# Performance work log

Hardware: AMD Instinct MI355X
Metric: run time of the kernel (lower is better)

## Reference

```python
import jax, jax.numpy as jnp
import numpy as np

B, S, H, I, E = 2, 2048, 1024, 4096, 8


def setup_inputs() -> dict:
    key = jax.random.key(0)
    k1, k2, k3, k4 = jax.random.split(key, 4)
    hidden_states = jax.random.normal(k1, (B, S, H), dtype=jnp.float32)
    # router: nn.Linear(H, E, bias=False) -> weight (E, H)
    Wr = jax.random.normal(k2, (E, H), dtype=jnp.float32) * 0.02
    # per-expert MLP: Linear(H,I) weight (I,H); Linear(I,H) weight (H,I); stacked over E
    W1 = jax.random.normal(k3, (E, I, H), dtype=jnp.float32) * 0.02
    W2 = jax.random.normal(k4, (E, H, I), dtype=jnp.float32) * 0.02
    return {"hidden_states": hidden_states, "Wr": Wr, "W1": W1, "W2": W2}


def reference(hidden_states, Wr, W1, W2):
    b, s, h = hidden_states.shape
    n_exp = Wr.shape[0]
    x = hidden_states.reshape(-1, h)                      # (N, H)
    logits = x @ Wr.T                                     # (N, E)
    probs = jax.nn.softmax(logits, axis=-1)               # (N, E)
    # top_k with k == num_experts: sorted probs descending (one-hot mask then
    # covers every expert, so each expert sees every token; expert i's output is
    # weighted by the i-th largest prob, exactly as the torch code does).
    top_probs, _ = jax.lax.top_k(probs, n_exp)            # (N, E)
    hmid = jnp.einsum('nh,eih->nei', x, W1)               # (N, E, I)
    hmid = jax.nn.gelu(hmid, approximate=False)           # exact erf GELU (torch nn.GELU default)
    yexp = jnp.einsum('nei,ehi->neh', hmid, W2)           # (N, E, H)
    out = jnp.einsum('neh,ne->nh', yexp, top_probs)       # weighted combine
    return out.reshape(b, s, h)
```

## Files before the change

kernel.cpp:

```cpp
#include <hip/hip_runtime.h>
#include <hip/hip_bf16.h>

#define NTOK 4096
#define HD   1024
#define ID   4096
#define NE   8
#define LDH  (NE * ID)

typedef float  floatx4 __attribute__((ext_vector_type(4)));
typedef __bf16 bf16x8  __attribute__((ext_vector_type(8)));
typedef unsigned short u16;

__device__ __forceinline__ u16 f2bf(float f) {
    union { float f; unsigned int i; } c; c.f = f;
    return (u16)((c.i + 0x7fffu + ((c.i >> 16) & 1u)) >> 16);
}

__device__ __forceinline__ void async_copy16(u16* lds, const u16* g) {
    __builtin_amdgcn_global_load_lds(
        (const __attribute__((address_space(1))) void*)g,
        (__attribute__((address_space(3))) void*)lds, 16, 0, 0);
}

__device__ __forceinline__ float gelu_fast(float v) {
    const float u = v * (0.7978845608f + 0.0356774081f * v * v);
    const float t = 1.f - 2.f / (__expf(2.f * u) + 1.f);
    return 0.5f * v * (1.f + t);
}

__global__ __launch_bounds__(256) void convert_kernel(
    const float* __restrict__ src, u16* __restrict__ dst)
{
    const size_t i = ((size_t)blockIdx.x * 256 + threadIdx.x) * 8;
    const float4 a = *(const float4*)(src + i);
    const float4 b = *(const float4*)(src + i + 4);
    ushort4 o0, o1;
    o0.x = f2bf(a.x); o0.y = f2bf(a.y); o0.z = f2bf(a.z); o0.w = f2bf(a.w);
    o1.x = f2bf(b.x); o1.y = f2bf(b.y); o1.z = f2bf(b.z); o1.w = f2bf(b.w);
    *(ushort4*)(dst + i)     = o0;
    *(ushort4*)(dst + i + 4) = o1;
}

__global__ __launch_bounds__(256) void router_kernel(
    const float* __restrict__ x, const float* __restrict__ Wr,
    float* __restrict__ wbuf)
{
    const int n    = blockIdx.x * 4 + (threadIdx.x >> 6);
    const int lane = threadIdx.x & 63;
    const float* xr = x + (size_t)n * HD;
    float acc[NE];
#pragma unroll
    for (int e = 0; e < NE; ++e) acc[e] = 0.f;
    for (int h = lane; h < HD; h += 64) {
        const float xv = xr[h];
#pragma unroll
        for (int e = 0; e < NE; ++e) acc[e] += xv * Wr[e * HD + h];
    }
#pragma unroll
    for (int e = 0; e < NE; ++e) {
        float v = acc[e];
#pragma unroll
        for (int off = 32; off > 0; off >>= 1) v += __shfl_xor(v, off, 64);
        acc[e] = v;
    }
    float mx = acc[0];
#pragma unroll
    for (int e = 1; e < NE; ++e) mx = fmaxf(mx, acc[e]);
    float s = 0.f;
#pragma unroll
    for (int e = 0; e < NE; ++e) { acc[e] = __expf(acc[e] - mx); s += acc[e]; }
    const float inv = 1.f / s;
#pragma unroll
    for (int e = 0; e < NE; ++e) acc[e] *= inv;
#pragma unroll
    for (int i = 0; i < NE - 1; ++i)
#pragma unroll
        for (int j = 0; j < NE - 1 - i; ++j) {
            const float a = acc[j], b = acc[j + 1];
            acc[j] = fmaxf(a, b); acc[j + 1] = fminf(a, b);
        }
    if (lane < NE) wbuf[lane * NTOK + n] = acc[lane];
}

__device__ __forceinline__ void gemm_tile(
    const u16* __restrict__ A, const u16* __restrict__ B,
    int ldA, int ldB, int kb, int ke, int rowBase, int colBase,
    u16* As, u16* Bs, floatx4 acc[4][4])
{
    const int t    = threadIdx.x;
    const int w    = t >> 6;
    const int lane = t & 63;
    const int wm   = w & 1, wn = w >> 1;
    const int quad = lane >> 4, l15 = lane & 15;
    const int srow = lane >> 2;
    const int scol = (lane & 3) << 3;

    const u16* gA = A + (size_t)(rowBase + w * 16 + srow) * ldA + kb + scol;
    const u16* gB = B + (size_t)(colBase + w * 16 + srow) * ldB + kb + scol;
    u16* ldsA = As + w * 512;
    u16* ldsB = Bs + w * 512;
    const size_t rstepA = (size_t)64 * ldA;
    const size_t rstepB = (size_t)64 * ldB;

    int aoff[4], boff[4];
#pragma unroll
    for (int i = 0; i < 4; ++i) {
        aoff[i] = (wm * 64 + i * 16 + l15) * 32 + quad * 8;
        boff[i] = (wn * 64 + i * 16 + l15) * 32 + quad * 8;
    }

    for (int k0 = kb; k0 < ke; k0 += 32) {
        async_copy16(ldsA,         gA);
        async_copy16(ldsA + 2048,  gA + rstepA);
        async_copy16(ldsB,         gB);
        async_copy16(ldsB + 2048,  gB + rstepB);
        gA += 32; gB += 32;
        __syncthreads();
        bf16x8 af[4], bfr[4];
#pragma unroll
        for (int i = 0; i < 4; ++i) {
            af[i]  = *(const bf16x8*)(As + aoff[i]);
            bfr[i] = *(const bf16x8*)(Bs + boff[i]);
        }
#pragma unroll
        for (int mi = 0; mi < 4; ++mi)
#pragma unroll
            for (int ni = 0; ni < 4; ++ni)
                acc[mi][ni] = __builtin_amdgcn_mfma_f32_16x16x32_bf16(
                    af[mi], bfr[ni], acc[mi][ni], 0, 0, 0);
        __syncthreads();
    }
}

__global__ __launch_bounds__(256) void gemm1_kernel(
    const u16* __restrict__ X, const u16* __restrict__ W1b,
    const float* __restrict__ wbuf, u16* __restrict__ hmid)
{
    __shared__ __align__(16) u16 As[128 * 32];
    __shared__ __align__(16) u16 Bs[128 * 32];
    floatx4 acc[4][4] = {};
    const int rowBase = blockIdx.y * 128, colBase = blockIdx.x * 128;
    const int e = colBase >> 12;
    gemm_tile(X, W1b, HD, HD, 0, HD, rowBase, colBase, As, Bs, acc);

    const int t = threadIdx.x, w = t >> 6, lane = t & 63;
    const int wm = w & 1, wn = w >> 1, quad = lane >> 4, l15 = lane & 15;
#pragma unroll
    for (int mi = 0; mi < 4; ++mi)
#pragma unroll
        for (int r = 0; r < 4; ++r) {
            const int row = rowBase + wm * 64 + mi * 16 + quad * 4 + r;
            const float wv = wbuf[e * NTOK + row];
#pragma unroll
            for (int ni = 0; ni < 4; ++ni) {
                const int col = colBase + wn * 64 + ni * 16 + l15;
                const float v = gelu_fast(acc[mi][ni][r]);
                hmid[(size_t)row * LDH + col] = f2bf(v * wv);
            }
        }
}

__global__ __launch_bounds__(256) void gemm2_kernel(
    const u16* __restrict__ hmid, const u16* __restrict__ W2b,
    float* __restrict__ accbuf)
{
    __shared__ __align__(16) u16 As[128 * 32];
    __shared__ __align__(16) u16 Bs[128 * 32];
    floatx4 acc[4][4] = {};
    const int rowBase = blockIdx.x * 128;
    const int colBase = blockIdx.y * 128;
    const int z = blockIdx.z;
    for (int ee = 0; ee < 2; ++ee) {
        const int e = 2 * z + ee;
        gemm_tile(hmid + (size_t)e * ID, W2b + (size_t)e * HD * ID,
                  LDH, ID, 0, ID, rowBase, colBase, As, Bs, acc);
    }

    float* accs = accbuf + (size_t)z * NTOK * HD;
    const int t = threadIdx.x, w = t >> 6, lane = t & 63;
    const int wm = w & 1, wn = w >> 1, quad = lane >> 4, l15 = lane & 15;
#pragma unroll
    for (int mi = 0; mi < 4; ++mi)
#pragma unroll
        for (int r = 0; r < 4; ++r) {
            const int row = rowBase + wm * 64 + mi * 16 + quad * 4 + r;
#pragma unroll
            for (int ni = 0; ni < 4; ++ni) {
                const int col = colBase + wn * 64 + ni * 16 + l15;
                accs[(size_t)row * HD + col] = acc[mi][ni][r];
            }
        }
}

__global__ __launch_bounds__(256) void finalize_kernel(
    const float* __restrict__ accbuf, float* __restrict__ out)
{
    const size_t NH = (size_t)NTOK * HD;
    const size_t i = ((size_t)blockIdx.x * 256 + threadIdx.x) * 4;
    const float4 a = *(const float4*)(accbuf + i);
    const float4 b = *(const float4*)(accbuf + NH + i);
    const float4 c = *(const float4*)(accbuf + 2 * NH + i);
    const float4 d = *(const float4*)(accbuf + 3 * NH + i);
    float4 o;
    o.x = a.x + b.x + c.x + d.x; o.y = a.y + b.y + c.y + d.y;
    o.z = a.z + b.z + c.z + d.z; o.w = a.w + b.w + c.w + d.w;
    *(float4*)(out + i) = o;
}

extern "C" void kernel_launch(void* const* d_in, const int* in_sizes, int n_in,
                              void* d_out, int out_size, void* d_ws, size_t ws_size,
                              hipStream_t stream) {
    const float* x  = (const float*)d_in[0];
    const float* Wr = (const float*)d_in[1];
    const float* W1 = (const float*)d_in[2];
    const float* W2 = (const float*)d_in[3];
    float* out = (float*)d_out;

    const size_t MB = 1024 * 1024;
    char* ws = (char*)d_ws;
    float* wbuf   = (float*)ws;
    u16*   Xb     = (u16*)(ws + 131072);
    u16*   W1b    = (u16*)(ws + 131072 + 8 * MB);
    u16*   W2b    = (u16*)(ws + 131072 + 72 * MB);
    u16*   hmid   = (u16*)(ws + 131072 + 136 * MB);
    float* accbuf = (float*)(ws + 131072 + 392 * MB);
    if (ws_size < 131072 + 456 * MB) return;

    convert_kernel<<<dim3((NTOK * HD) / 2048), 256, 0, stream>>>(x, Xb);
    convert_kernel<<<dim3((NE * ID * HD) / 2048), 256, 0, stream>>>(W1, W1b);
    convert_kernel<<<dim3((NE * HD * ID) / 2048), 256, 0, stream>>>(W2, W2b);
    router_kernel<<<dim3(NTOK / 4), 256, 0, stream>>>(x, Wr, wbuf);

    gemm1_kernel<<<dim3(NE * ID / 128, NTOK / 128), 256, 0, stream>>>(
        Xb, W1b, wbuf, hmid);
    gemm2_kernel<<<dim3(NTOK / 128, HD / 128, 4), 256, 0, stream>>>(
        hmid, W2b, accbuf);
    finalize_kernel<<<dim3(NTOK * HD / 1024), 256, 0, stream>>>(accbuf, out);
}
```

Baseline: 1.167 ms.

## Stage gemm1 epilogue through LDS, use per-expert hmid layout, split gemm2 per expert

```diff
diff --git a/kernel.cpp b/kernel.cpp
--- a/kernel.cpp
+++ b/kernel.cpp
@@ -5,7 +5,6 @@
 #define HD   1024
 #define ID   4096
 #define NE   8
-#define LDH  (NE * ID)
 
 typedef float  floatx4 __attribute__((ext_vector_type(4)));
 typedef __bf16 bf16x8  __attribute__((ext_vector_type(8)));
@@ -84,7 +83,7 @@
 
 __device__ __forceinline__ void gemm_tile(
     const u16* __restrict__ A, const u16* __restrict__ B,
-    int ldA, int ldB, int kb, int ke, int rowBase, int colBase,
+    int ldA, int ldB, int K, int rowBase, int colBase,
     u16* As, u16* Bs, floatx4 acc[4][4])
 {
     const int t    = threadIdx.x;
@@ -95,8 +94,8 @@
     const int srow = lane >> 2;
     const int scol = (lane & 3) << 3;
 
-    const u16* gA = A + (size_t)(rowBase + w * 16 + srow) * ldA + kb + scol;
-    const u16* gB = B + (size_t)(colBase + w * 16 + srow) * ldB + kb + scol;
+    const u16* gA = A + (size_t)(rowBase + w * 16 + srow) * ldA + scol;
+    const u16* gB = B + (size_t)(colBase + w * 16 + srow) * ldB + scol;
     u16* ldsA = As + w * 512;
     u16* ldsB = Bs + w * 512;
     const size_t rstepA = (size_t)64 * ldA;
@@ -109,7 +108,7 @@
         boff[i] = (wn * 64 + i * 16 + l15) * 32 + quad * 8;
     }
 
-    for (int k0 = kb; k0 < ke; k0 += 32) {
+    for (int k0 = 0; k0 < K; k0 += 32) {
         async_copy16(ldsA,         gA);
         async_copy16(ldsA + 2048,  gA + rstepA);
         async_copy16(ldsB,         gB);
@@ -132,16 +131,19 @@
     }
 }
 
+#define TSTRIDE 136
 __global__ __launch_bounds__(256) void gemm1_kernel(
     const u16* __restrict__ X, const u16* __restrict__ W1b,
     const float* __restrict__ wbuf, u16* __restrict__ hmid)
 {
-    __shared__ __align__(16) u16 As[128 * 32];
-    __shared__ __align__(16) u16 Bs[128 * 32];
+    __shared__ __align__(16) u16 smem[128 * TSTRIDE];
+    u16* As = smem;
+    u16* Bs = smem + 4096;
     floatx4 acc[4][4] = {};
     const int rowBase = blockIdx.y * 128, colBase = blockIdx.x * 128;
-    const int e = colBase >> 12;
-    gemm_tile(X, W1b, HD, HD, 0, HD, rowBase, colBase, As, Bs, acc);
+    const int e = blockIdx.x >> 5;
+    const int colLocal = colBase & (ID - 1);
+    gemm_tile(X, W1b, HD, HD, HD, rowBase, colBase, As, Bs, acc);
 
     const int t = threadIdx.x, w = t >> 6, lane = t & 63;
     const int wm = w & 1, wn = w >> 1, quad = lane >> 4, l15 = lane & 15;
@@ -149,15 +151,23 @@
     for (int mi = 0; mi < 4; ++mi)
 #pragma unroll
         for (int r = 0; r < 4; ++r) {
-            const int row = rowBase + wm * 64 + mi * 16 + quad * 4 + r;
-            const float wv = wbuf[e * NTOK + row];
+            const int row = wm * 64 + mi * 16 + quad * 4 + r;
+            const float wv = wbuf[e * NTOK + rowBase + row];
 #pragma unroll
             for (int ni = 0; ni < 4; ++ni) {
-                const int col = colBase + wn * 64 + ni * 16 + l15;
-                const float v = gelu_fast(acc[mi][ni][r]);
-                hmid[(size_t)row * LDH + col] = f2bf(v * wv);
+                const int col = wn * 64 + ni * 16 + l15;
+                smem[row * TSTRIDE + col] = f2bf(gelu_fast(acc[mi][ni][r]) * wv);
             }
         }
+    __syncthreads();
+    u16* hmidE = hmid + (size_t)e * NTOK * ID;
+    const int c0 = (t & 15) * 8;
+#pragma unroll
+    for (int p = 0; p < 8; ++p) {
+        const int row = p * 16 + (t >> 4);
+        const bf16x8 v = *(const bf16x8*)(smem + row * TSTRIDE + c0);
+        *(bf16x8*)(hmidE + (size_t)(rowBase + row) * ID + colLocal + c0) = v;
+    }
 }
 
 __global__ __launch_bounds__(256) void gemm2_kernel(
@@ -169,14 +179,11 @@
     floatx4 acc[4][4] = {};
     const int rowBase = blockIdx.x * 128;
     const int colBase = blockIdx.y * 128;
-    const int z = blockIdx.z;
-    for (int ee = 0; ee < 2; ++ee) {
-        const int e = 2 * z + ee;
-        gemm_tile(hmid + (size_t)e * ID, W2b + (size_t)e * HD * ID,
-                  LDH, ID, 0, ID, rowBase, colBase, As, Bs, acc);
-    }
-
-    float* accs = accbuf + (size_t)z * NTOK * HD;
+    const int e = blockIdx.z;
+    gemm_tile(hmid + (size_t)e * NTOK * ID, W2b + (size_t)e * HD * ID,
+              ID, ID, ID, rowBase, colBase, As, Bs, acc);
+
+    float* accs = accbuf + (size_t)e * NTOK * HD;
     const int t = threadIdx.x, w = t >> 6, lane = t & 63;
     const int wm = w & 1, wn = w >> 1, quad = lane >> 4, l15 = lane & 15;
 #pragma unroll
@@ -197,13 +204,12 @@
 {
     const size_t NH = (size_t)NTOK * HD;
     const size_t i = ((size_t)blockIdx.x * 256 + threadIdx.x) * 4;
-    const float4 a = *(const float4*)(accbuf + i);
-    const float4 b = *(const float4*)(accbuf + NH + i);
-    const float4 c = *(const float4*)(accbuf + 2 * NH + i);
-    const float4 d = *(const float4*)(accbuf + 3 * NH + i);
-    float4 o;
-    o.x = a.x + b.x + c.x + d.x; o.y = a.y + b.y + c.y + d.y;
-    o.z = a.z + b.z + c.z + d.z; o.w = a.w + b.w + c.w + d.w;
+    float4 o = *(const float4*)(accbuf + i);
+#pragma unroll
+    for (int z = 1; z < NE; ++z) {
+        const float4 a = *(const float4*)(accbuf + z * NH + i);
+        o.x += a.x; o.y += a.y; o.z += a.z; o.w += a.w;
+    }
     *(float4*)(out + i) = o;
 }
 
@@ -220,10 +226,10 @@
     char* ws = (char*)d_ws;
     float* wbuf   = (float*)ws;
     u16*   Xb     = (u16*)(ws + 131072);
-    u16*   W1b    = (u16*)(ws + 131072 + 8 * MB);
-    u16*   W2b    = (u16*)(ws + 131072 + 72 * MB);
-    u16*   hmid   = (u16*)(ws + 131072 + 136 * MB);
-    float* accbuf = (float*)(ws + 131072 + 392 * MB);
+    u16*   W2b    = (u16*)(ws + 131072 + 8 * MB);
+    u16*   hmid   = (u16*)(ws + 131072 + 72 * MB);
+    u16*   W1b    = (u16*)(ws + 131072 + 328 * MB);
+    float* accbuf = (float*)(ws + 131072 + 328 * MB);
     if (ws_size < 131072 + 456 * MB) return;
 
     convert_kernel<<<dim3((NTOK * HD) / 2048), 256, 0, stream>>>(x, Xb);
@@ -233,7 +239,7 @@
 
     gemm1_kernel<<<dim3(NE * ID / 128, NTOK / 128), 256, 0, stream>>>(
         Xb, W1b, wbuf, hmid);
-    gemm2_kernel<<<dim3(NTOK / 128, HD / 128, 4), 256, 0, stream>>>(
+    gemm2_kernel<<<dim3(NTOK / 128, HD / 128, NE), 256, 0, stream>>>(
         hmid, W2b, accbuf);
     finalize_kernel<<<dim3(NTOK * HD / 1024), 256, 0, stream>>>(accbuf, out);
 }
```

Result: no change. 1.178 ms (+1.0%).
